# Performance work log

Hardware: AMD Instinct MI355X
Metric: run time of the kernel (lower is better)

The kernel has to match this reference:

```python
import jax, jax.numpy as jnp
import numpy as np

B, S, E, H, FF = 8, 1024, 1024, 16, 4096
DK = E // H
EPS = 1.1920929e-07  # torch RMSNorm default eps = finfo(float32).eps


def _rmsnorm(x, g):
    return x * jax.lax.rsqrt(jnp.mean(x * x, axis=-1, keepdims=True) + EPS) * g


def _rope(q, k):
    # q, k: [B, H, S, DK]; standard rotate-half RoPE, theta=10000
    d = q.shape[-1]
    s = q.shape[-2]
    inv_freq = 1.0 / (10000.0 ** (jnp.arange(0, d, 2, dtype=jnp.float32) / d))
    ang = jnp.arange(s, dtype=jnp.float32)[:, None] * inv_freq  # [S, d/2]
    cos = jnp.concatenate([jnp.cos(ang), jnp.cos(ang)], axis=-1)  # [S, d]
    sin = jnp.concatenate([jnp.sin(ang), jnp.sin(ang)], axis=-1)

    def rot(x):
        x1, x2 = jnp.split(x, 2, axis=-1)
        return jnp.concatenate([-x2, x1], axis=-1)

    return q * cos + rot(q) * sin, k * cos + rot(k) * sin


def setup_inputs() -> dict:
    key = jax.random.key(0)
    ks = jax.random.split(key, 16)
    sc = 0.02
    inp = {
        "x": jax.random.normal(ks[0], (B, S, E), dtype=jnp.float32),
        "WQ": jax.random.normal(ks[1], (E, E), dtype=jnp.float32) * sc,
        "bQ": jnp.zeros((E,), jnp.float32),
        "WK": jax.random.normal(ks[2], (E, E), dtype=jnp.float32) * sc,
        "bK": jnp.zeros((E,), jnp.float32),
        "WV": jax.random.normal(ks[3], (E, E), dtype=jnp.float32) * sc,
        "bV": jnp.zeros((E,), jnp.float32),
        "WO": jax.random.normal(ks[4], (E, E), dtype=jnp.float32) * sc,
        "bO": jnp.zeros((E,), jnp.float32),
        "W1": jax.random.normal(ks[5], (E, FF), dtype=jnp.float32) * sc,
        "b1": jnp.zeros((FF,), jnp.float32),
        "W2": jax.random.normal(ks[6], (FF, E), dtype=jnp.float32) * sc,
        "b2": jnp.zeros((E,), jnp.float32),
        "g1": jnp.ones((E,), jnp.float32),
        "g2": jnp.ones((E,), jnp.float32),
    }
    return inp


def reference(x, WQ, bQ, WK, bK, WV, bV, WO, bO, W1, b1, W2, b2, g1, g2):
    b, s, e = x.shape

    def attn(h):
        q = (h @ WQ + bQ).reshape(b, s, H, DK).transpose(0, 2, 1, 3)
        k = (h @ WK + bK).reshape(b, s, H, DK).transpose(0, 2, 1, 3)
        v = (h @ WV + bV).reshape(b, s, H, DK).transpose(0, 2, 1, 3)
        q, k = _rope(q, k)
        scores = jnp.einsum("bhqd,bhkd->bhqk", q, k) / jnp.sqrt(jnp.float32(DK))
        p = jax.nn.softmax(scores, axis=-1)
        o = jnp.einsum("bhqk,bhkd->bhqd", p, v)
        o = o.transpose(0, 2, 1, 3).reshape(b, s, e)
        return o @ WO + bO

    def ffn(h):
        return jax.nn.relu(h @ W1 + b1) @ W2 + b2

    x = x + attn(_rmsnorm(x, g1))
    x = x + ffn(_rmsnorm(x, g2))
    return x
```

## Files before the change

### kernel.cpp

```cpp
#include <hip/hip_runtime.h>
#include <math.h>

#define B_ 8
#define S_ 1024
#define E_ 1024
#define H_ 16
#define FF_ 4096

typedef __attribute__((ext_vector_type(8))) short bf16x8;
typedef __attribute__((ext_vector_type(4))) float f32x4;

#define QSCALE 0.1803368801111f
#define LG2_10K 0.4152410118f

__device__ __forceinline__ unsigned short f2bf(float f) {
  union { float f; unsigned u; } v;
  v.f = f;
  unsigned r = v.u + 0x7fffu + ((v.u >> 16) & 1u);
  return (unsigned short)(r >> 16);
}
__device__ __forceinline__ float bf2f(unsigned short u) {
  union { unsigned u; float f; } v;
  v.u = ((unsigned)u) << 16;
  return v.f;
}
__device__ __forceinline__ unsigned fbits(float f) {
  union { float f; unsigned u; } v;
  v.f = f;
  return v.u;
}

__device__ __forceinline__ void glds16(const void* g, void* l) {
  __builtin_amdgcn_global_load_lds(
      (const __attribute__((address_space(1))) unsigned int*)g,
      (__attribute__((address_space(3))) unsigned int*)l, 16, 0, 0);
}

__global__ __launch_bounds__(256) void wconvT(const float* __restrict__ W,
                                              unsigned short* __restrict__ Wt,
                                              int K, int N) {
  __shared__ float t[32][33];
  const int tx = threadIdx.x & 31, ty = threadIdx.x >> 5;
  const int n0 = blockIdx.x * 32, k0 = blockIdx.y * 32;
#pragma unroll
  for (int p = 0; p < 4; ++p)
    t[ty + p * 8][tx] = W[(size_t)(k0 + ty + p * 8) * N + n0 + tx];
  __syncthreads();
#pragma unroll
  for (int p = 0; p < 4; ++p)
    Wt[(size_t)(n0 + ty + p * 8) * K + k0 + tx] = f2bf(t[tx][ty + p * 8]);
}

__global__ __launch_bounds__(256) void wconvT4(const float* __restrict__ W0,
                                               const float* __restrict__ W1p,
                                               const float* __restrict__ W2p,
                                               const float* __restrict__ W3p,
                                               unsigned short* __restrict__ D0,
                                               unsigned short* __restrict__ D1,
                                               unsigned short* __restrict__ D2,
                                               unsigned short* __restrict__ D3) {
  __shared__ float t[32][33];
  const int z = blockIdx.z;
  const float* W = (z == 0) ? W0 : (z == 1) ? W1p : (z == 2) ? W2p : W3p;
  unsigned short* D = (z == 0) ? D0 : (z == 1) ? D1 : (z == 2) ? D2 : D3;
  const int tx = threadIdx.x & 31, ty = threadIdx.x >> 5;
  const int n0 = blockIdx.x * 32, k0 = blockIdx.y * 32;
#pragma unroll
  for (int p = 0; p < 4; ++p)
    t[ty + p * 8][tx] = W[(size_t)(k0 + ty + p * 8) * E_ + n0 + tx];
  __syncthreads();
#pragma unroll
  for (int p = 0; p < 4; ++p)
    D[(size_t)(n0 + ty + p * 8) * E_ + k0 + tx] = f2bf(t[tx][ty + p * 8]);
}

__global__ __launch_bounds__(256) void bpack(const float* __restrict__ bQ,
                                             const float* __restrict__ bK,
                                             const float* __restrict__ bV,
                                             float* __restrict__ o) {
  const int i = blockIdx.x * 256 + threadIdx.x;
  const float v = (i < 1024) ? bQ[i] : ((i < 2048) ? bK[i - 1024] : bV[i - 2048]);
  o[i] = v;
}

__global__ __launch_bounds__(256) void rmsnorm_kernel(const float* __restrict__ x,
                                                      const float* __restrict__ g,
                                                      unsigned short* __restrict__ out) {
  const int row = blockIdx.x;
  const int t = threadIdx.x;
  const float4 v = ((const float4*)(x + (size_t)row * E_))[t];
  float ss = v.x * v.x + v.y * v.y + v.z * v.z + v.w * v.w;
#pragma unroll
  for (int off = 32; off > 0; off >>= 1) ss += __shfl_down(ss, off);
  __shared__ float sred[4];
  if ((t & 63) == 0) sred[t >> 6] = ss;
  __syncthreads();
  const float tot = sred[0] + sred[1] + sred[2] + sred[3];
  const float rinv = rsqrtf(tot * (1.0f / E_) + 1.1920929e-07f);
  const float4 gv = ((const float4*)g)[t];
  ushort4 o;
  o.x = f2bf(v.x * rinv * gv.x);
  o.y = f2bf(v.y * rinv * gv.y);
  o.z = f2bf(v.z * rinv * gv.z);
  o.w = f2bf(v.w * rinv * gv.w);
  ((ushort4*)(out + (size_t)row * E_))[t] = o;
}

template <int OUT_BF16, int RELU, int RES>
__global__ __launch_bounds__(256) void gemm_bf16(const unsigned short* __restrict__ A,
                                                 const unsigned short* __restrict__ Bt,
                                                 const float* __restrict__ bias,
                                                 const float* __restrict__ res,
                                                 void* __restrict__ C,
                                                 int M, int N, int K) {
  __shared__ unsigned short As[128 * 32];
  __shared__ unsigned short Bs[128 * 32];
  const int tid = threadIdx.x;
  const int w = tid >> 6;
  const int lane = tid & 63;

  const int nb = gridDim.x;
  const int id = blockIdx.x;
  const int lid = (id & 7) * (nb >> 3) + (id >> 3);
  const int per = (M >> 7) * 8;
  const int grp = lid / per;
  const int rem = lid - grp * per;
  const int bn = (grp * 8 + (rem & 7)) * 128;
  const int bm = (rem >> 3) * 128;

  const int wm = (w & 1) * 64, wn = (w >> 1) * 64;

  f32x4 acc[4][4];
#pragma unroll
  for (int i = 0; i < 4; ++i)
#pragma unroll
    for (int j = 0; j < 4; ++j) acc[i][j] = (f32x4){0.f, 0.f, 0.f, 0.f};

  const unsigned short* Ap0 = A + (size_t)(bm + w * 32 + (lane >> 2)) * K + (lane & 3) * 8;
  const unsigned short* Ap1 = Ap0 + (size_t)16 * K;
  const unsigned short* Bp0 = Bt + (size_t)(bn + w * 32 + (lane >> 2)) * K + (lane & 3) * 8;
  const unsigned short* Bp1 = Bp0 + (size_t)16 * K;
  unsigned short* AsD0 = &As[w * 1024];
  unsigned short* AsD1 = AsD0 + 512;
  unsigned short* BsD0 = &Bs[w * 1024];
  unsigned short* BsD1 = BsD0 + 512;

  const int fr = lane & 15;
  const int fk = (lane >> 4) * 8;

  for (int k0 = 0; k0 < K; k0 += 32) {
    __syncthreads();
    glds16(Ap0 + k0, AsD0);
    glds16(Ap1 + k0, AsD1);
    glds16(Bp0 + k0, BsD0);
    glds16(Bp1 + k0, BsD1);
    __syncthreads();
    bf16x8 a[4], b[4];
#pragma unroll
    for (int im = 0; im < 4; ++im)
      a[im] = *(const bf16x8*)&As[(wm + im * 16 + fr) * 32 + fk];
#pragma unroll
    for (int in = 0; in < 4; ++in)
      b[in] = *(const bf16x8*)&Bs[(wn + in * 16 + fr) * 32 + fk];
#pragma unroll
    for (int im = 0; im < 4; ++im)
#pragma unroll
      for (int in = 0; in < 4; ++in)
        acc[im][in] = __builtin_amdgcn_mfma_f32_16x16x32_bf16(a[im], b[in], acc[im][in], 0, 0, 0);
  }

#pragma unroll
  for (int im = 0; im < 4; ++im) {
    const int row0 = bm + wm + im * 16 + (lane >> 4) * 4;
#pragma unroll
    for (int in = 0; in < 4; ++in) {
      const int col = bn + wn + in * 16 + (lane & 15);
      const float bv = bias[col];
#pragma unroll
      for (int r = 0; r < 4; ++r) {
        float v = acc[im][in][r] + bv;
        if (RES) v += res[(size_t)(row0 + r) * N + col];
        if (RELU) v = fmaxf(v, 0.0f);
        if (OUT_BF16)
          ((unsigned short*)C)[(size_t)(row0 + r) * N + col] = f2bf(v);
        else
          ((float*)C)[(size_t)(row0 + r) * N + col] = v;
      }
    }
  }
}

__global__ __launch_bounds__(256) void gemm_sk2(const unsigned short* __restrict__ A,
                                                const unsigned short* __restrict__ Bt,
                                                unsigned short* __restrict__ Pp) {
  const int N = 1024, K = 4096, KH = 2048;
  __shared__ unsigned short As[128 * 32];
  __shared__ unsigned short Bs[128 * 32];
  const int tid = threadIdx.x;
  const int w = tid >> 6;
  const int lane = tid & 63;

  const int id = blockIdx.x;
  const int kh = id >> 9;
  const int hid = id & 511;
  const int lid = (hid & 7) * 64 + (hid >> 3);
  const int bn = (lid & 7) * 128;
  const int bm = (lid >> 3) * 128;

  const int wm = (w & 1) * 64, wn = (w >> 1) * 64;

  f32x4 acc[4][4];
#pragma unroll
  for (int i = 0; i < 4; ++i)
#pragma unroll
    for (int j = 0; j < 4; ++j) acc[i][j] = (f32x4){0.f, 0.f, 0.f, 0.f};

  const unsigned short* Ap0 =
      A + (size_t)(bm + w * 32 + (lane >> 2)) * K + kh * KH + (lane & 3) * 8;
  const unsigned short* Ap1 = Ap0 + (size_t)16 * K;
  const unsigned short* Bp0 =
      Bt + (size_t)(bn + w * 32 + (lane >> 2)) * K + kh * KH + (lane & 3) * 8;
  const unsigned short* Bp1 = Bp0 + (size_t)16 * K;
  unsigned short* AsD0 = &As[w * 1024];
  unsigned short* AsD1 = AsD0 + 512;
  unsigned short* BsD0 = &Bs[w * 1024];
  unsigned short* BsD1 = BsD0 + 512;

  const int fr = lane & 15;
  const int fk = (lane >> 4) * 8;

  for (int k0 = 0; k0 < KH; k0 += 32) {
    __syncthreads();
    glds16(Ap0 + k0, AsD0);
    glds16(Ap1 + k0, AsD1);
    glds16(Bp0 + k0, BsD0);
    glds16(Bp1 + k0, BsD1);
    __syncthreads();
    bf16x8 a[4], b[4];
#pragma unroll
    for (int im = 0; im < 4; ++im)
      a[im] = *(const bf16x8*)&As[(wm + im * 16 + fr) * 32 + fk];
#pragma unroll
    for (int in = 0; in < 4; ++in)
      b[in] = *(const bf16x8*)&Bs[(wn + in * 16 + fr) * 32 + fk];
#pragma unroll
    for (int im = 0; im < 4; ++im)
#pragma unroll
      for (int in = 0; in < 4; ++in)
        acc[im][in] = __builtin_amdgcn_mfma_f32_16x16x32_bf16(a[im], b[in], acc[im][in], 0, 0, 0);
  }

  unsigned short* P = Pp + (size_t)kh * (8u << 20);
#pragma unroll
  for (int im = 0; im < 4; ++im) {
    const int row0 = bm + wm + im * 16 + (lane >> 4) * 4;
#pragma unroll
    for (int in = 0; in < 4; ++in) {
      const int col = bn + wn + in * 16 + fr;
#pragma unroll
      for (int r = 0; r < 4; ++r)
        P[(size_t)(row0 + r) * N + col] = f2bf(acc[im][in][r]);
    }
  }
}

__global__ __launch_bounds__(256) void ff2_reduce(const unsigned short* __restrict__ Pp,
                                                  const float* __restrict__ x1,
                                                  const float* __restrict__ b2,
                                                  float* __restrict__ out) {
  const int i = blockIdx.x * 256 + threadIdx.x;
  const size_t off = (size_t)i * 4;
  const ushort4 p0 = *(const ushort4*)(Pp + off);
  const ushort4 p1 = *(const ushort4*)(Pp + (8u << 20) + off);
  const float4 xv = *(const float4*)(x1 + off);
  const float4 bv = *(const float4*)(b2 + (off & 1023));
  float4 o;
  o.x = xv.x + bv.x + bf2f(p0.x) + bf2f(p1.x);
  o.y = xv.y + bv.y + bf2f(p0.y) + bf2f(p1.y);
  o.z = xv.z + bv.z + bf2f(p0.z) + bf2f(p1.z);
  o.w = xv.w + bv.w + bf2f(p0.w) + bf2f(p1.w);
  *(float4*)(out + off) = o;
}

template <int OUT_BF16, int RELU, int RES>
__global__ __launch_bounds__(256) void gemm_n64(const unsigned short* __restrict__ A,
                                                const unsigned short* __restrict__ Bt,
                                                const float* __restrict__ bias,
                                                const float* __restrict__ res,
                                                void* __restrict__ C,
                                                int M, int N, int K) {
  __shared__ unsigned short As[128 * 32];
  __shared__ unsigned short Bs[64 * 32];
  const int tid = threadIdx.x;
  const int w = tid >> 6;
  const int lane = tid & 63;

  const int nbn = N >> 6;
  const int bm = (blockIdx.x / nbn) * 128;
  const int bn = (blockIdx.x % nbn) * 64;

  const int wm = (w & 1) * 64, wn = (w >> 1) * 32;

  f32x4 acc[4][2];
#pragma unroll
  for (int i = 0; i < 4; ++i)
#pragma unroll
    for (int j = 0; j < 2; ++j) acc[i][j] = (f32x4){0.f, 0.f, 0.f, 0.f};

  const unsigned short* Ap0 = A + (size_t)(bm + w * 32 + (lane >> 2)) * K + (lane & 3) * 8;
  const unsigned short* Ap1 = Ap0 + (size_t)16 * K;
  const unsigned short* Bp0 = Bt + (size_t)(bn + w * 16 + (lane >> 2)) * K + (lane & 3) * 8;
  unsigned short* AsD0 = &As[w * 1024];
  unsigned short* AsD1 = AsD0 + 512;
  unsigned short* BsD0 = &Bs[w * 512];

  const int fr = lane & 15;
  const int fk = (lane >> 4) * 8;

  for (int k0 = 0; k0 < K; k0 += 32) {
    __syncthreads();
    glds16(Ap0 + k0, AsD0);
    glds16(Ap1 + k0, AsD1);
    glds16(Bp0 + k0, BsD0);
    __syncthreads();
    bf16x8 a[4], b[2];
#pragma unroll
    for (int im = 0; im < 4; ++im)
      a[im] = *(const bf16x8*)&As[(wm + im * 16 + fr) * 32 + fk];
#pragma unroll
    for (int in = 0; in < 2; ++in)
      b[in] = *(const bf16x8*)&Bs[(wn + in * 16 + fr) * 32 + fk];
#pragma unroll
    for (int im = 0; im < 4; ++im)
#pragma unroll
      for (int in = 0; in < 2; ++in)
        acc[im][in] = __builtin_amdgcn_mfma_f32_16x16x32_bf16(a[im], b[in], acc[im][in], 0, 0, 0);
  }

#pragma unroll
  for (int im = 0; im < 4; ++im) {
    const int row0 = bm + wm + im * 16 + (lane >> 4) * 4;
#pragma unroll
    for (int in = 0; in < 2; ++in) {
      const int col = bn + wn + in * 16 + fr;
      const float bv = bias[col];
#pragma unroll
      for (int r = 0; r < 4; ++r) {
        float v = acc[im][in][r] + bv;
        if (RES) v += res[(size_t)(row0 + r) * N + col];
        if (RELU) v = fmaxf(v, 0.0f);
        if (OUT_BF16)
          ((unsigned short*)C)[(size_t)(row0 + r) * N + col] = f2bf(v);
        else
          ((float*)C)[(size_t)(row0 + r) * N + col] = v;
      }
    }
  }
}

__global__ __launch_bounds__(256) void gemm_qkv(const unsigned short* __restrict__ A,
                                                const unsigned short* __restrict__ Bt,
                                                const float* __restrict__ bias,
                                                unsigned short* __restrict__ QKV,
                                                unsigned short* __restrict__ Vt,
                                                int M, int K) {
  const int N = 3072;
  __shared__ unsigned short As[128 * 32];
  __shared__ unsigned short Bs[128 * 32];
  const int tid = threadIdx.x;
  const int w = tid >> 6;
  const int lane = tid & 63;

  const int nb = gridDim.x;
  const int id = blockIdx.x;
  const int lid = (id & 7) * (nb >> 3) + (id >> 3);
  const int per = (M >> 7) * 8;
  const int grp = lid / per;
  const int rem = lid - grp * per;
  const int bn = (grp * 8 + (rem & 7)) * 128;
  const int bm = (rem >> 3) * 128;

  const int wm = (w & 1) * 64, wn = (w >> 1) * 64;

  f32x4 acc[4][4];
#pragma unroll
  for (int i = 0; i < 4; ++i)
#pragma unroll
    for (int j = 0; j < 4; ++j) acc[i][j] = (f32x4){0.f, 0.f, 0.f, 0.f};

  const unsigned short* Ap0 = A + (size_t)(bm + w * 32 + (lane >> 2)) * K + (lane & 3) * 8;
  const unsigned short* Ap1 = Ap0 + (size_t)16 * K;
  const unsigned short* Bp0 = Bt + (size_t)(bn + w * 32 + (lane >> 2)) * K + (lane & 3) * 8;
  const unsigned short* Bp1 = Bp0 + (size_t)16 * K;
  unsigned short* AsD0 = &As[w * 1024];
  unsigned short* AsD1 = AsD0 + 512;
  unsigned short* BsD0 = &Bs[w * 1024];
  unsigned short* BsD1 = BsD0 + 512;

  const int fr = lane & 15;
  const int fk = (lane >> 4) * 8;

  for (int k0 = 0; k0 < K; k0 += 32) {
    __syncthreads();
    glds16(Ap0 + k0, AsD0);
    glds16(Ap1 + k0, AsD1);
    glds16(Bp0 + k0, BsD0);
    glds16(Bp1 + k0, BsD1);
    __syncthreads();
    bf16x8 a[4], b[4];
#pragma unroll
    for (int im = 0; im < 4; ++im)
      a[im] = *(const bf16x8*)&As[(wm + im * 16 + fr) * 32 + fk];
#pragma unroll
    for (int in = 0; in < 4; ++in)
      b[in] = *(const bf16x8*)&Bs[(wn + in * 16 + fr) * 32 + fk];
#pragma unroll
    for (int im = 0; im < 4; ++im)
#pragma unroll
      for (int in = 0; in < 4; ++in)
        acc[im][in] = __builtin_amdgcn_mfma_f32_16x16x32_bf16(a[im], b[in], acc[im][in], 0, 0, 0);
  }

  const int cbase = bn + wn;
  const int seg = cbase >> 6;
  const int typ = seg >> 4;
  const int hh = seg & 15;
  const int bidx = bm >> 10;
  float bv[4];
#pragma unroll
  for (int in = 0; in < 4; ++in) bv[in] = bias[cbase + in * 16 + fr];

  if (typ == 2) {
#pragma unroll
    for (int im = 0; im < 4; ++im) {
      const int s0 = (bm & 1023) + wm + im * 16 + (lane >> 4) * 4;
#pragma unroll
      for (int in = 0; in < 4; ++in) {
        const int d = in * 16 + fr;
        ushort4 o4;
        o4.x = f2bf(acc[im][in][0] + bv[in]);
        o4.y = f2bf(acc[im][in][1] + bv[in]);
        o4.z = f2bf(acc[im][in][2] + bv[in]);
        o4.w = f2bf(acc[im][in][3] + bv[in]);
        *(ushort4*)&Vt[(size_t)((bidx * 16 + hh) * 64 + d) * S_ + s0] = o4;
      }
    }
  } else {
    const float qs = (typ == 0) ? QSCALE : 1.0f;
    const float i0 = exp2f(-LG2_10K * (float)fr);
    const float i1 = exp2f(-LG2_10K * (float)(fr + 16));
#pragma unroll
    for (int im = 0; im < 4; ++im) {
      const int row0 = bm + wm + im * 16 + (lane >> 4) * 4;
#pragma unroll
      for (int r = 0; r < 4; ++r) {
        const int row = row0 + r;
        const float s = (float)(row & 1023);
        float sn0, cs0, sn1, cs1;
        __sincosf(s * i0, &sn0, &cs0);
        __sincosf(s * i1, &sn1, &cs1);
        const float x0 = acc[im][0][r] + bv[0];
        const float x1 = acc[im][1][r] + bv[1];
        const float x2 = acc[im][2][r] + bv[2];
        const float x3 = acc[im][3][r] + bv[3];
        unsigned short* cp = QKV + (size_t)row * 3072 + cbase;
        cp[fr]      = f2bf((x0 * cs0 - x2 * sn0) * qs);
        cp[16 + fr] = f2bf((x1 * cs1 - x3 * sn1) * qs);
        cp[32 + fr] = f2bf((x2 * cs0 + x0 * sn0) * qs);
        cp[48 + fr] = f2bf((x3 * cs1 + x1 * sn1) * qs);
      }
    }
  }
}

__global__ __launch_bounds__(256) void attn_v4(const unsigned short* __restrict__ QKV,
                                               const unsigned short* __restrict__ Vt,
                                               unsigned short* __restrict__ Og) {
  __shared__ unsigned short Kf[2][8 * 512];
  __shared__ unsigned short Vf[2][8 * 512];
  __shared__ unsigned short Ps[4][32 * 72];
  const int tid = threadIdx.x;
  const int w = tid >> 6, lane = tid & 63;
  const int qt = blockIdx.x, bh = blockIdx.y;
  const int b = bh >> 4, h = bh & 15;
  const int fr = lane & 15, g = lane >> 4, fk = g * 8;
  const int q0w = qt * 128 + w * 32;

  bf16x8 qB[2][2];
#pragma unroll
  for (int nt = 0; nt < 2; ++nt)
#pragma unroll
    for (int c = 0; c < 2; ++c)
      qB[nt][c] = *(const bf16x8*)&QKV[(size_t)(b * S_ + q0w + nt * 16 + fr) * 3072 +
                                       h * 64 + c * 32 + fk];

  f32x4 o[4][2];
#pragma unroll
  for (int mt = 0; mt < 4; ++mt)
#pragma unroll
    for (int nt = 0; nt < 2; ++nt) o[mt][nt] = (f32x4){0.f, 0.f, 0.f, 0.f};
  float l[2] = {0.0f, 0.0f};

#define STAGE(kt, bufi)                                                                   \
  {                                                                                       \
    _Pragma("unroll") for (int p = 0; p < 4; ++p) {                                       \
      const int u = w * 4 + p;                                                            \
      if (u < 8) {                                                                        \
        const int mt = u >> 1, c = u & 1;                                                 \
        glds16(QKV + (size_t)(b * S_ + (kt) * 64 + mt * 16 + fr) * 3072 + 1024 + h * 64 + \
                   c * 32 + fk,                                                           \
               &Kf[bufi][u * 512]);                                                       \
      } else {                                                                            \
        const int v2 = u - 8, mt = v2 >> 1, c = v2 & 1;                                   \
        glds16(Vt + (size_t)(bh * 64 + mt * 16 + fr) * S_ + (kt) * 64 + c * 32 + fk,      \
               &Vf[bufi][v2 * 512]);                                                      \
      }                                                                                   \
    }                                                                                     \
  }

  STAGE(0, 0);

  for (int kt = 0; kt < 16; ++kt) {
    __syncthreads();
    if (kt < 15) STAGE(kt + 1, (kt + 1) & 1);
    const unsigned short* Kc = Kf[kt & 1];
    const unsigned short* Vc = Vf[kt & 1];

    f32x4 s[4][2];
#pragma unroll
    for (int mt = 0; mt < 4; ++mt) {
      const bf16x8 k0 = *(const bf16x8*)&Kc[(mt * 2 + 0) * 512 + lane * 8];
      const bf16x8 k1 = *(const bf16x8*)&Kc[(mt * 2 + 1) * 512 + lane * 8];
#pragma unroll
      for (int nt = 0; nt < 2; ++nt) {
        f32x4 a = (f32x4){0.f, 0.f, 0.f, 0.f};
        a = __builtin_amdgcn_mfma_f32_16x16x32_bf16(k0, qB[nt][0], a, 0, 0, 0);
        a = __builtin_amdgcn_mfma_f32_16x16x32_bf16(k1, qB[nt][1], a, 0, 0, 0);
        s[mt][nt] = a;
      }
    }

#pragma unroll
    for (int nt = 0; nt < 2; ++nt) {
      float rs = 0.0f;
#pragma unroll
      for (int mt = 0; mt < 4; ++mt)
#pragma unroll
        for (int r = 0; r < 4; ++r) {
          const float p = exp2f(s[mt][nt][r]);
          s[mt][nt][r] = p;
          rs += p;
        }
      rs += __shfl_xor(rs, 16);
      rs += __shfl_xor(rs, 32);
      l[nt] += rs;
    }

#pragma unroll
    for (int nt = 0; nt < 2; ++nt)
#pragma unroll
      for (int mt = 0; mt < 4; ++mt) {
        uint2 pk;
        pk.x = __builtin_amdgcn_perm(fbits(s[mt][nt][1]), fbits(s[mt][nt][0]), 0x07060302u);
        pk.y = __builtin_amdgcn_perm(fbits(s[mt][nt][3]), fbits(s[mt][nt][2]), 0x07060302u);
        *(uint2*)&Ps[w][(nt * 16 + fr) * 72 + mt * 16 + g * 4] = pk;
      }

    bf16x8 pB[2][2];
#pragma unroll
    for (int nt = 0; nt < 2; ++nt)
#pragma unroll
      for (int c = 0; c < 2; ++c)
        pB[nt][c] = *(const bf16x8*)&Ps[w][(nt * 16 + fr) * 72 + c * 32 + fk];
#pragma unroll
    for (int mt = 0; mt < 4; ++mt) {
      const bf16x8 v0 = *(const bf16x8*)&Vc[(mt * 2 + 0) * 512 + lane * 8];
      const bf16x8 v1 = *(const bf16x8*)&Vc[(mt * 2 + 1) * 512 + lane * 8];
#pragma unroll
      for (int nt = 0; nt < 2; ++nt) {
        o[mt][nt] = __builtin_amdgcn_mfma_f32_16x16x32_bf16(v0, pB[nt][0], o[mt][nt], 0, 0, 0);
        o[mt][nt] = __builtin_amdgcn_mfma_f32_16x16x32_bf16(v1, pB[nt][1], o[mt][nt], 0, 0, 0);
      }
    }
  }

  const float linv0 = 1.0f / l[0], linv1 = 1.0f / l[1];
#pragma unroll
  for (int nt = 0; nt < 2; ++nt) {
    const float li = nt ? linv1 : linv0;
#pragma unroll
    for (int mt = 0; mt < 4; ++mt) {
      uint2 pk;
      pk.x = __builtin_amdgcn_perm(fbits(o[mt][nt][1] * li), fbits(o[mt][nt][0] * li), 0x07060302u);
      pk.y = __builtin_amdgcn_perm(fbits(o[mt][nt][3] * li), fbits(o[mt][nt][2] * li), 0x07060302u);
      *(uint2*)&Ps[w][(nt * 16 + fr) * 72 + mt * 16 + g * 4] = pk;
    }
  }
  const int qr = lane >> 1, hf = lane & 1;
#pragma unroll
  for (int c = 0; c < 2; ++c) {
    const bf16x8 vv = *(const bf16x8*)&Ps[w][qr * 72 + hf * 16 + c * 32];
    *(bf16x8*)&Og[(size_t)(b * S_ + q0w + qr) * E_ + h * 64 + hf * 16 + c * 32] = vv;
  }
}

extern "C" void kernel_launch(void* const* d_in, const int* in_sizes, int n_in,
                              void* d_out, int out_size, void* d_ws, size_t ws_size,
                              hipStream_t stream) {
  const float* x  = (const float*)d_in[0];
  const float* WQ = (const float*)d_in[1];
  const float* bQ = (const float*)d_in[2];
  const float* WK = (const float*)d_in[3];
  const float* bK = (const float*)d_in[4];
  const float* WV = (const float*)d_in[5];
  const float* bV = (const float*)d_in[6];
  const float* WO = (const float*)d_in[7];
  const float* bO = (const float*)d_in[8];
  const float* W1 = (const float*)d_in[9];
  const float* b1 = (const float*)d_in[10];
  const float* W2 = (const float*)d_in[11];
  const float* b2 = (const float*)d_in[12];
  const float* g1 = (const float*)d_in[13];
  const float* g2 = (const float*)d_in[14];
  float* out = (float*)d_out;

  char* ws = (char*)d_ws;
  const size_t MB = 1024 * 1024;
  unsigned short* h1   = (unsigned short*)(ws + 0 * MB);
  unsigned short* QKV  = (unsigned short*)(ws + 16 * MB);
  unsigned short* Vt   = (unsigned short*)(ws + 64 * MB);
  unsigned short* Ob   = (unsigned short*)(ws + 80 * MB);
  float*          x1   = (float*)(ws + 96 * MB);
  unsigned short* h2   = (unsigned short*)(ws + 128 * MB);
  unsigned short* mid  = (unsigned short*)(ws + 16 * MB);
  unsigned short* WQKVt= (unsigned short*)(ws + 144 * MB);
  unsigned short* WOt  = (unsigned short*)(ws + 150 * MB);
  unsigned short* W1t  = (unsigned short*)(ws + 152 * MB);
  unsigned short* W2t  = (unsigned short*)(ws + 160 * MB);
  float*          bqkv = (float*)(ws + 168 * MB);
  unsigned short* Pp   = (unsigned short*)(ws + 176 * MB);

  const int M = B_ * S_;

  wconvT4<<<dim3(32, 32, 4), 256, 0, stream>>>(WQ, WK, WV, WO, WQKVt,
                                               WQKVt + 1024 * 1024,
                                               WQKVt + 2 * 1024 * 1024, WOt);
  wconvT<<<dim3(128, 32), 256, 0, stream>>>(W1, W1t, E_, FF_);
  wconvT<<<dim3(32, 128), 256, 0, stream>>>(W2, W2t, FF_, E_);
  bpack<<<12, 256, 0, stream>>>(bQ, bK, bV, bqkv);

  rmsnorm_kernel<<<M, 256, 0, stream>>>(x, g1, h1);

  gemm_qkv<<<24 * 64, 256, 0, stream>>>(h1, WQKVt, bqkv, QKV, Vt, M, E_);

  attn_v4<<<dim3(8, B_ * H_), 256, 0, stream>>>(QKV, Vt, Ob);

  gemm_n64<0, 0, 1><<<64 * 16, 256, 0, stream>>>(Ob, WOt, bO, x, x1, M, E_, E_);

  rmsnorm_kernel<<<M, 256, 0, stream>>>(x1, g2, h2);

  gemm_bf16<1, 1, 0><<<32 * 64, 256, 0, stream>>>(h2, W1t, b1, nullptr, mid, M, FF_, E_);

  gemm_sk2<<<1024, 256, 0, stream>>>(mid, W2t, Pp);

  ff2_reduce<<<8192, 256, 0, stream>>>(Pp, x1, b2, out);
}
```

Baseline: 537.7 us.

## Double GEMM K-tile to 64 with XOR-swizzled LDS and merge prep kernels

```diff
diff --git a/kernel.cpp b/kernel.cpp
--- a/kernel.cpp
+++ b/kernel.cpp
@@ -36,51 +36,55 @@
       (__attribute__((address_space(3))) unsigned int*)l, 16, 0, 0);
 }
 
-__global__ __launch_bounds__(256) void wconvT(const float* __restrict__ W,
-                                              unsigned short* __restrict__ Wt,
-                                              int K, int N) {
+__global__ __launch_bounds__(256) void prep(const float* __restrict__ WQ,
+                                            const float* __restrict__ WK,
+                                            const float* __restrict__ WV,
+                                            const float* __restrict__ WO,
+                                            const float* __restrict__ W1,
+                                            const float* __restrict__ W2,
+                                            const float* __restrict__ bQ,
+                                            const float* __restrict__ bK,
+                                            const float* __restrict__ bV,
+                                            unsigned short* __restrict__ WQKVt,
+                                            unsigned short* __restrict__ WOt,
+                                            unsigned short* __restrict__ W1t,
+                                            unsigned short* __restrict__ W2t,
+                                            float* __restrict__ bqkv) {
+  const int id = blockIdx.x;
+  if (id >= 12288) {
+    const int i = (id - 12288) * 256 + threadIdx.x;
+    if (i < 3072)
+      bqkv[i] = (i < 1024) ? bQ[i] : ((i < 2048) ? bK[i - 1024] : bV[i - 2048]);
+    return;
+  }
+  const float* W;
+  unsigned short* D;
+  int K, N, x, y;
+  if (id < 4096) {
+    const int m = id >> 10;
+    const float* ws4[4] = {WQ, WK, WV, WO};
+    unsigned short* ds4[4] = {WQKVt, WQKVt + 1024 * 1024, WQKVt + 2 * 1024 * 1024, WOt};
+    W = ws4[m]; D = ds4[m]; K = 1024; N = 1024;
+    x = id & 31; y = (id >> 5) & 31;
+  } else if (id < 8192) {
+    const int j = id - 4096;
+    W = W1; D = W1t; K = 1024; N = 4096;
+    x = j & 127; y = j >> 7;
+  } else {
+    const int j = id - 8192;
+    W = W2; D = W2t; K = 4096; N = 1024;
+    x = j & 31; y = j >> 5;
+  }
   __shared__ float t[32][33];
   const int tx = threadIdx.x & 31, ty = threadIdx.x >> 5;
-  const int n0 = blockIdx.x * 32, k0 = blockIdx.y * 32;
+  const int n0 = x * 32, k0 = y * 32;
 #pragma unroll
   for (int p = 0; p < 4; ++p)
     t[ty + p * 8][tx] = W[(size_t)(k0 + ty + p * 8) * N + n0 + tx];
   __syncthreads();
 #pragma unroll
   for (int p = 0; p < 4; ++p)
-    Wt[(size_t)(n0 + ty + p * 8) * K + k0 + tx] = f2bf(t[tx][ty + p * 8]);
-}
-
-__global__ __launch_bounds__(256) void wconvT4(const float* __restrict__ W0,
-                                               const float* __restrict__ W1p,
-                                               const float* __restrict__ W2p,
-                                               const float* __restrict__ W3p,
-                                               unsigned short* __restrict__ D0,
-                                               unsigned short* __restrict__ D1,
-                                               unsigned short* __restrict__ D2,
-                                               unsigned short* __restrict__ D3) {
-  __shared__ float t[32][33];
-  const int z = blockIdx.z;
-  const float* W = (z == 0) ? W0 : (z == 1) ? W1p : (z == 2) ? W2p : W3p;
-  unsigned short* D = (z == 0) ? D0 : (z == 1) ? D1 : (z == 2) ? D2 : D3;
-  const int tx = threadIdx.x & 31, ty = threadIdx.x >> 5;
-  const int n0 = blockIdx.x * 32, k0 = blockIdx.y * 32;
-#pragma unroll
-  for (int p = 0; p < 4; ++p)
-    t[ty + p * 8][tx] = W[(size_t)(k0 + ty + p * 8) * E_ + n0 + tx];
-  __syncthreads();
-#pragma unroll
-  for (int p = 0; p < 4; ++p)
-    D[(size_t)(n0 + ty + p * 8) * E_ + k0 + tx] = f2bf(t[tx][ty + p * 8]);
-}
-
-__global__ __launch_bounds__(256) void bpack(const float* __restrict__ bQ,
-                                             const float* __restrict__ bK,
-                                             const float* __restrict__ bV,
-                                             float* __restrict__ o) {
-  const int i = blockIdx.x * 256 + threadIdx.x;
-  const float v = (i < 1024) ? bQ[i] : ((i < 2048) ? bK[i - 1024] : bV[i - 2048]);
-  o[i] = v;
+    D[(size_t)(n0 + ty + p * 8) * K + k0 + tx] = f2bf(t[tx][ty + p * 8]);
 }
 
 __global__ __launch_bounds__(256) void rmsnorm_kernel(const float* __restrict__ x,
@@ -106,6 +110,7 @@
   ((ushort4*)(out + (size_t)row * E_))[t] = o;
 }
 
+
 template <int OUT_BF16, int RELU, int RES>
 __global__ __launch_bounds__(256) void gemm_bf16(const unsigned short* __restrict__ A,
                                                  const unsigned short* __restrict__ Bt,
@@ -113,8 +118,8 @@
                                                  const float* __restrict__ res,
                                                  void* __restrict__ C,
                                                  int M, int N, int K) {
-  __shared__ unsigned short As[128 * 32];
-  __shared__ unsigned short Bs[128 * 32];
+  __shared__ unsigned short As[128 * 64];
+  __shared__ unsigned short Bs[128 * 64];
   const int tid = threadIdx.x;
   const int w = tid >> 6;
   const int lane = tid & 63;
@@ -136,37 +141,50 @@
 #pragma unroll
     for (int j = 0; j < 4; ++j) acc[i][j] = (f32x4){0.f, 0.f, 0.f, 0.f};
 
-  const unsigned short* Ap0 = A + (size_t)(bm + w * 32 + (lane >> 2)) * K + (lane & 3) * 8;
-  const unsigned short* Ap1 = Ap0 + (size_t)16 * K;
-  const unsigned short* Bp0 = Bt + (size_t)(bn + w * 32 + (lane >> 2)) * K + (lane & 3) * 8;
-  const unsigned short* Bp1 = Bp0 + (size_t)16 * K;
-  unsigned short* AsD0 = &As[w * 1024];
-  unsigned short* AsD1 = AsD0 + 512;
-  unsigned short* BsD0 = &Bs[w * 1024];
-  unsigned short* BsD1 = BsD0 + 512;
+  const int srow = lane >> 3;
+  const int skb = (lane & 7) ^ srow;
+  const unsigned short* Ap[4];
+  const unsigned short* Bp[4];
+  unsigned short* AsD[4];
+  unsigned short* BsD[4];
+#pragma unroll
+  for (int p = 0; p < 4; ++p) {
+    const int u = w * 4 + p;
+    Ap[p] = A + (size_t)(bm + u * 8 + srow) * K + skb * 8;
+    Bp[p] = Bt + (size_t)(bn + u * 8 + srow) * K + skb * 8;
+    AsD[p] = &As[u * 512 + lane * 8];
+    BsD[p] = &Bs[u * 512 + lane * 8];
+  }
 
   const int fr = lane & 15;
-  const int fk = (lane >> 4) * 8;
-
-  for (int k0 = 0; k0 < K; k0 += 32) {
-    __syncthreads();
-    glds16(Ap0 + k0, AsD0);
-    glds16(Ap1 + k0, AsD1);
-    glds16(Bp0 + k0, BsD0);
-    glds16(Bp1 + k0, BsD1);
-    __syncthreads();
-    bf16x8 a[4], b[4];
+  const int g = lane >> 4;
+  const int sw = fr & 7;
+
+  for (int k0 = 0; k0 < K; k0 += 64) {
+    __syncthreads();
+#pragma unroll
+    for (int p = 0; p < 4; ++p) glds16(Ap[p] + k0, AsD[p]);
+#pragma unroll
+    for (int p = 0; p < 4; ++p) glds16(Bp[p] + k0, BsD[p]);
+    __syncthreads();
+    bf16x8 a[4][2], b[4][2];
 #pragma unroll
     for (int im = 0; im < 4; ++im)
-      a[im] = *(const bf16x8*)&As[(wm + im * 16 + fr) * 32 + fk];
+#pragma unroll
+      for (int kc = 0; kc < 2; ++kc)
+        a[im][kc] = *(const bf16x8*)&As[(wm + im * 16 + fr) * 64 + ((kc * 4 + g) ^ sw) * 8];
 #pragma unroll
     for (int in = 0; in < 4; ++in)
-      b[in] = *(const bf16x8*)&Bs[(wn + in * 16 + fr) * 32 + fk];
+#pragma unroll
+      for (int kc = 0; kc < 2; ++kc)
+        b[in][kc] = *(const bf16x8*)&Bs[(wn + in * 16 + fr) * 64 + ((kc * 4 + g) ^ sw) * 8];
 #pragma unroll
     for (int im = 0; im < 4; ++im)
 #pragma unroll
-      for (int in = 0; in < 4; ++in)
-        acc[im][in] = __builtin_amdgcn_mfma_f32_16x16x32_bf16(a[im], b[in], acc[im][in], 0, 0, 0);
+      for (int in = 0; in < 4; ++in) {
+        acc[im][in] = __builtin_amdgcn_mfma_f32_16x16x32_bf16(a[im][0], b[in][0], acc[im][in], 0, 0, 0);
+        acc[im][in] = __builtin_amdgcn_mfma_f32_16x16x32_bf16(a[im][1], b[in][1], acc[im][in], 0, 0, 0);
+      }
   }
 
 #pragma unroll
@@ -174,7 +192,7 @@
     const int row0 = bm + wm + im * 16 + (lane >> 4) * 4;
 #pragma unroll
     for (int in = 0; in < 4; ++in) {
-      const int col = bn + wn + in * 16 + (lane & 15);
+      const int col = bn + wn + in * 16 + fr;
       const float bv = bias[col];
 #pragma unroll
       for (int r = 0; r < 4; ++r) {
@@ -194,8 +212,8 @@
                                                 const unsigned short* __restrict__ Bt,
                                                 unsigned short* __restrict__ Pp) {
   const int N = 1024, K = 4096, KH = 2048;
-  __shared__ unsigned short As[128 * 32];
-  __shared__ unsigned short Bs[128 * 32];
+  __shared__ unsigned short As[128 * 64];
+  __shared__ unsigned short Bs[128 * 64];
   const int tid = threadIdx.x;
   const int w = tid >> 6;
   const int lane = tid & 63;
@@ -215,39 +233,50 @@
 #pragma unroll
     for (int j = 0; j < 4; ++j) acc[i][j] = (f32x4){0.f, 0.f, 0.f, 0.f};
 
-  const unsigned short* Ap0 =
-      A + (size_t)(bm + w * 32 + (lane >> 2)) * K + kh * KH + (lane & 3) * 8;
-  const unsigned short* Ap1 = Ap0 + (size_t)16 * K;
-  const unsigned short* Bp0 =
-      Bt + (size_t)(bn + w * 32 + (lane >> 2)) * K + kh * KH + (lane & 3) * 8;
-  const unsigned short* Bp1 = Bp0 + (size_t)16 * K;
-  unsigned short* AsD0 = &As[w * 1024];
-  unsigned short* AsD1 = AsD0 + 512;
-  unsigned short* BsD0 = &Bs[w * 1024];
-  unsigned short* BsD1 = BsD0 + 512;
+  const int srow = lane >> 3;
+  const int skb = (lane & 7) ^ srow;
+  const unsigned short* Ap[4];
+  const unsigned short* Bp[4];
+  unsigned short* AsD[4];
+  unsigned short* BsD[4];
+#pragma unroll
+  for (int p = 0; p < 4; ++p) {
+    const int u = w * 4 + p;
+    Ap[p] = A + (size_t)(bm + u * 8 + srow) * K + kh * KH + skb * 8;
+    Bp[p] = Bt + (size_t)(bn + u * 8 + srow) * K + kh * KH + skb * 8;
+    AsD[p] = &As[u * 512 + lane * 8];
+    BsD[p] = &Bs[u * 512 + lane * 8];
+  }
 
   const int fr = lane & 15;
-  const int fk = (lane >> 4) * 8;
-
-  for (int k0 = 0; k0 < KH; k0 += 32) {
-    __syncthreads();
-    glds16(Ap0 + k0, AsD0);
-    glds16(Ap1 + k0, AsD1);
-    glds16(Bp0 + k0, BsD0);
-    glds16(Bp1 + k0, BsD1);
-    __syncthreads();
-    bf16x8 a[4], b[4];
+  const int g = lane >> 4;
+  const int sw = fr & 7;
+
+  for (int k0 = 0; k0 < KH; k0 += 64) {
+    __syncthreads();
+#pragma unroll
+    for (int p = 0; p < 4; ++p) glds16(Ap[p] + k0, AsD[p]);
+#pragma unroll
+    for (int p = 0; p < 4; ++p) glds16(Bp[p] + k0, BsD[p]);
+    __syncthreads();
+    bf16x8 a[4][2], b[4][2];
 #pragma unroll
     for (int im = 0; im < 4; ++im)
-      a[im] = *(const bf16x8*)&As[(wm + im * 16 + fr) * 32 + fk];
+#pragma unroll
+      for (int kc = 0; kc < 2; ++kc)
+        a[im][kc] = *(const bf16x8*)&As[(wm + im * 16 + fr) * 64 + ((kc * 4 + g) ^ sw) * 8];
 #pragma unroll
     for (int in = 0; in < 4; ++in)
-      b[in] = *(const bf16x8*)&Bs[(wn + in * 16 + fr) * 32 + fk];
+#pragma unroll
+      for (int kc = 0; kc < 2; ++kc)
+        b[in][kc] = *(const bf16x8*)&Bs[(wn + in * 16 + fr) * 64 + ((kc * 4 + g) ^ sw) * 8];
 #pragma unroll
     for (int im = 0; im < 4; ++im)
 #pragma unroll
-      for (int in = 0; in < 4; ++in)
-        acc[im][in] = __builtin_amdgcn_mfma_f32_16x16x32_bf16(a[im], b[in], acc[im][in], 0, 0, 0);
+      for (int in = 0; in < 4; ++in) {
+        acc[im][in] = __builtin_amdgcn_mfma_f32_16x16x32_bf16(a[im][0], b[in][0], acc[im][in], 0, 0, 0);
+        acc[im][in] = __builtin_amdgcn_mfma_f32_16x16x32_bf16(a[im][1], b[in][1], acc[im][in], 0, 0, 0);
+      }
   }
 
   unsigned short* P = Pp + (size_t)kh * (8u << 20);
@@ -289,8 +318,8 @@
                                                 const float* __restrict__ res,
                                                 void* __restrict__ C,
                                                 int M, int N, int K) {
-  __shared__ unsigned short As[128 * 32];
-  __shared__ unsigned short Bs[64 * 32];
+  __shared__ unsigned short As[128 * 64];
+  __shared__ unsigned short Bs[64 * 64];
   const int tid = threadIdx.x;
   const int w = tid >> 6;
   const int lane = tid & 63;
@@ -307,34 +336,54 @@
 #pragma unroll
     for (int j = 0; j < 2; ++j) acc[i][j] = (f32x4){0.f, 0.f, 0.f, 0.f};
 
-  const unsigned short* Ap0 = A + (size_t)(bm + w * 32 + (lane >> 2)) * K + (lane & 3) * 8;
-  const unsigned short* Ap1 = Ap0 + (size_t)16 * K;
-  const unsigned short* Bp0 = Bt + (size_t)(bn + w * 16 + (lane >> 2)) * K + (lane & 3) * 8;
-  unsigned short* AsD0 = &As[w * 1024];
-  unsigned short* AsD1 = AsD0 + 512;
-  unsigned short* BsD0 = &Bs[w * 512];
+  const int srow = lane >> 3;
+  const int skb = (lane & 7) ^ srow;
+  const unsigned short* Ap[4];
+  const unsigned short* Bp[2];
+  unsigned short* AsD[4];
+  unsigned short* BsD[2];
+#pragma unroll
+  for (int p = 0; p < 4; ++p) {
+    const int u = w * 4 + p;
+    Ap[p] = A + (size_t)(bm + u * 8 + srow) * K + skb * 8;
+    AsD[p] = &As[u * 512 + lane * 8];
+  }
+#pragma unroll
+  for (int p = 0; p < 2; ++p) {
+    const int u = w * 2 + p;
+    Bp[p] = Bt + (size_t)(bn + u * 8 + srow) * K + skb * 8;
+    BsD[p] = &Bs[u * 512 + lane * 8];
+  }
 
   const int fr = lane & 15;
-  const int fk = (lane >> 4) * 8;
-
-  for (int k0 = 0; k0 < K; k0 += 32) {
-    __syncthreads();
-    glds16(Ap0 + k0, AsD0);
-    glds16(Ap1 + k0, AsD1);
-    glds16(Bp0 + k0, BsD0);
-    __syncthreads();
-    bf16x8 a[4], b[2];
+  const int g = lane >> 4;
+  const int sw = fr & 7;
+
+  for (int k0 = 0; k0 < K; k0 += 64) {
+    __syncthreads();
+#pragma unroll
+    for (int p = 0; p < 4; ++p) glds16(Ap[p] + k0, AsD[p]);
+#pragma unroll
+    for (int p = 0; p < 2; ++p) glds16(Bp[p] + k0, BsD[p]);
+    __syncthreads();
+    bf16x8 a[4][2], b[2][2];
 #pragma unroll
     for (int im = 0; im < 4; ++im)
-      a[im] = *(const bf16x8*)&As[(wm + im * 16 + fr) * 32 + fk];
+#pragma unroll
+      for (int kc = 0; kc < 2; ++kc)
+        a[im][kc] = *(const bf16x8*)&As[(wm + im * 16 + fr) * 64 + ((kc * 4 + g) ^ sw) * 8];
 #pragma unroll
     for (int in = 0; in < 2; ++in)
-      b[in] = *(const bf16x8*)&Bs[(wn + in * 16 + fr) * 32 + fk];
+#pragma unroll
+      for (int kc = 0; kc < 2; ++kc)
+        b[in][kc] = *(const bf16x8*)&Bs[(wn + in * 16 + fr) * 64 + ((kc * 4 + g) ^ sw) * 8];
 #pragma unroll
     for (int im = 0; im < 4; ++im)
 #pragma unroll
-      for (int in = 0; in < 2; ++in)
-        acc[im][in] = __builtin_amdgcn_mfma_f32_16x16x32_bf16(a[im], b[in], acc[im][in], 0, 0, 0);
+      for (int in = 0; in < 2; ++in) {
+        acc[im][in] = __builtin_amdgcn_mfma_f32_16x16x32_bf16(a[im][0], b[in][0], acc[im][in], 0, 0, 0);
+        acc[im][in] = __builtin_amdgcn_mfma_f32_16x16x32_bf16(a[im][1], b[in][1], acc[im][in], 0, 0, 0);
+      }
   }
 
 #pragma unroll
@@ -364,9 +413,8 @@
                                                 unsigned short* __restrict__ QKV,
                                                 unsigned short* __restrict__ Vt,
                                                 int M, int K) {
-  const int N = 3072;
-  __shared__ unsigned short As[128 * 32];
-  __shared__ unsigned short Bs[128 * 32];
+  __shared__ unsigned short As[128 * 64];
+  __shared__ unsigned short Bs[128 * 64];
   const int tid = threadIdx.x;
   const int w = tid >> 6;
   const int lane = tid & 63;
@@ -388,37 +436,50 @@
 #pragma unroll
     for (int j = 0; j < 4; ++j) acc[i][j] = (f32x4){0.f, 0.f, 0.f, 0.f};
 
-  const unsigned short* Ap0 = A + (size_t)(bm + w * 32 + (lane >> 2)) * K + (lane & 3) * 8;
-  const unsigned short* Ap1 = Ap0 + (size_t)16 * K;
-  const unsigned short* Bp0 = Bt + (size_t)(bn + w * 32 + (lane >> 2)) * K + (lane & 3) * 8;
-  const unsigned short* Bp1 = Bp0 + (size_t)16 * K;
-  unsigned short* AsD0 = &As[w * 1024];
-  unsigned short* AsD1 = AsD0 + 512;
-  unsigned short* BsD0 = &Bs[w * 1024];
-  unsigned short* BsD1 = BsD0 + 512;
+  const int srow = lane >> 3;
+  const int skb = (lane & 7) ^ srow;
+  const unsigned short* Ap[4];
+  const unsigned short* Bp[4];
+  unsigned short* AsD[4];
+  unsigned short* BsD[4];
+#pragma unroll
+  for (int p = 0; p < 4; ++p) {
+    const int u = w * 4 + p;
+    Ap[p] = A + (size_t)(bm + u * 8 + srow) * K + skb * 8;
+    Bp[p] = Bt + (size_t)(bn + u * 8 + srow) * K + skb * 8;
+    AsD[p] = &As[u * 512 + lane * 8];
+    BsD[p] = &Bs[u * 512 + lane * 8];
+  }
 
   const int fr = lane & 15;
-  const int fk = (lane >> 4) * 8;
-
-  for (int k0 = 0; k0 < K; k0 += 32) {
-    __syncthreads();
-    glds16(Ap0 + k0, AsD0);
-    glds16(Ap1 + k0, AsD1);
-    glds16(Bp0 + k0, BsD0);
-    glds16(Bp1 + k0, BsD1);
-    __syncthreads();
-    bf16x8 a[4], b[4];
+  const int g = lane >> 4;
+  const int sw = fr & 7;
+
+  for (int k0 = 0; k0 < K; k0 += 64) {
+    __syncthreads();
+#pragma unroll
+    for (int p = 0; p < 4; ++p) glds16(Ap[p] + k0, AsD[p]);
+#pragma unroll
+    for (int p = 0; p < 4; ++p) glds16(Bp[p] + k0, BsD[p]);
+    __syncthreads();
+    bf16x8 a[4][2], b[4][2];
 #pragma unroll
     for (int im = 0; im < 4; ++im)
-      a[im] = *(const bf16x8*)&As[(wm + im * 16 + fr) * 32 + fk];
+#pragma unroll
+      for (int kc = 0; kc < 2; ++kc)
+        a[im][kc] = *(const bf16x8*)&As[(wm + im * 16 + fr) * 64 + ((kc * 4 + g) ^ sw) * 8];
 #pragma unroll
     for (int in = 0; in < 4; ++in)
-      b[in] = *(const bf16x8*)&Bs[(wn + in * 16 + fr) * 32 + fk];
+#pragma unroll
+      for (int kc = 0; kc < 2; ++kc)
+        b[in][kc] = *(const bf16x8*)&Bs[(wn + in * 16 + fr) * 64 + ((kc * 4 + g) ^ sw) * 8];
 #pragma unroll
     for (int im = 0; im < 4; ++im)
 #pragma unroll
-      for (int in = 0; in < 4; ++in)
-        acc[im][in] = __builtin_amdgcn_mfma_f32_16x16x32_bf16(a[im], b[in], acc[im][in], 0, 0, 0);
+      for (int in = 0; in < 4; ++in) {
+        acc[im][in] = __builtin_amdgcn_mfma_f32_16x16x32_bf16(a[im][0], b[in][0], acc[im][in], 0, 0, 0);
+        acc[im][in] = __builtin_amdgcn_mfma_f32_16x16x32_bf16(a[im][1], b[in][1], acc[im][in], 0, 0, 0);
+      }
   }
 
   const int cbase = bn + wn;
@@ -642,12 +703,8 @@
 
   const int M = B_ * S_;
 
-  wconvT4<<<dim3(32, 32, 4), 256, 0, stream>>>(WQ, WK, WV, WO, WQKVt,
-                                               WQKVt + 1024 * 1024,
-                                               WQKVt + 2 * 1024 * 1024, WOt);
-  wconvT<<<dim3(128, 32), 256, 0, stream>>>(W1, W1t, E_, FF_);
-  wconvT<<<dim3(32, 128), 256, 0, stream>>>(W2, W2t, FF_, E_);
-  bpack<<<12, 256, 0, stream>>>(bQ, bK, bV, bqkv);
+  prep<<<12300, 256, 0, stream>>>(WQ, WK, WV, WO, W1, W2, bQ, bK, bV,
+                                  WQKVt, WOt, W1t, W2t, bqkv);
 
   rmsnorm_kernel<<<M, 256, 0, stream>>>(x, g1, h1);
 
```

Result: faster. 495.2 us (-7.9%).
